# Kernel tuning notes

Measured on AMD Instinct MI355X. Metric: run time of the kernel, lower is better.

## Reference

```python
import jax, jax.numpy as jnp
import numpy as np

E = 64          # moe_num_experts
H = 1024        # hidden_size
F = 2816        # per_expert_ff_dim
T = 4096        # total tokens (equal split: 64 per expert)


def setup_inputs() -> dict:
    key = jax.random.key(0)
    k1, k2, k3, k4 = jax.random.split(key, 4)
    s = 1.0 / np.sqrt(H)
    return {
        "x": jax.random.normal(k1, (T, H), dtype=jnp.float32),
        "tokens_per_expert": jnp.full((E,), T // E, dtype=jnp.int32),
        "w1": jax.random.normal(k2, (E * F, H), dtype=jnp.float32) * s,
        "w3": jax.random.normal(k3, (E * F, H), dtype=jnp.float32) * s,
        "w2": jax.random.normal(k4, (E * F, H), dtype=jnp.float32) * s,
    }


def reference(x, tokens_per_expert, w1, w3, w2):
    # Tokens are grouped contiguously per expert with an equal split,
    # so the variable-size grouped GEMM (gg.ops.gmm) reduces to a batched einsum.
    tpe = x.shape[0] // E
    xg = x.reshape(E, tpe, H)            # [E, t, h]
    w1e = w1.reshape(E, F, H)
    w3e = w3.reshape(E, F, H)
    w2e = w2.reshape(E, F, H)
    # gmm(x, w1, trans_b=True): per-expert x @ w1[e].T
    h1 = jnp.einsum("eth,efh->etf", xg, w1e)   # [E, t, f]
    h3 = jnp.einsum("eth,efh->etf", xg, w3e)   # [E, t, f]
    gated = jax.nn.silu(h1) * h3               # SwiGLU
    # gmm(gated, w2): per-expert gated @ w2[e]  ([t,f] @ [f,h])
    out = jnp.einsum("etf,efh->eth", gated, w2e)
    return out.reshape(-1, H)
```

## Files before the change

kernel.cpp:

```cpp
#include <hip/hip_runtime.h>
#include <hip/hip_bf16.h>

#define NE   64
#define NH   1024
#define NF   2816
#define TPE  64
#define PITCH 72

typedef __attribute__((ext_vector_type(8))) short bf16x8;
typedef __attribute__((ext_vector_type(4))) float f32x4;

__device__ __forceinline__ ushort f2bf(float f) {
    union { float f; unsigned u; } v; v.f = f;
    unsigned r = v.u + 0x7fffu + ((v.u >> 16) & 1u);
    return (ushort)(r >> 16);
}

__device__ __forceinline__ bf16x8 cvt8(f32x4 lo, f32x4 hi) {
    bf16x8 r;
    #pragma unroll
    for (int j = 0; j < 4; ++j) {
        r[j]     = (short)f2bf(lo[j]);
        r[4 + j] = (short)f2bf(hi[j]);
    }
    return r;
}

#define GLOAD16(gsrc, ldst)                                                          \
    __builtin_amdgcn_global_load_lds(                                                \
        (const __attribute__((address_space(1))) void*)(gsrc),                       \
        (__attribute__((address_space(3))) void*)(ldst), 16, 0, 0)

__global__ __launch_bounds__(256)
void xcast(const float* __restrict__ x, ushort* __restrict__ xb) {
    const int i = blockIdx.x * 256 + threadIdx.x;
    const f32x4 a = *(const f32x4*)(x + (size_t)i * 8);
    const f32x4 b = *(const f32x4*)(x + (size_t)i * 8 + 4);
    *(bf16x8*)(xb + (size_t)i * 8) = cvt8(a, b);
}

__global__ __launch_bounds__(256, 4)
void k1_gate(const ushort* __restrict__ xb,
             const float* __restrict__ w1,
             const float* __restrict__ w3,
             ushort* __restrict__ g) {
    __shared__ float fbuf[10240];
    ushort* lX  = (ushort*)fbuf;
    float*  lW1 = fbuf + 2048;
    float*  lW3 = fbuf + 6144;

    const int e    = blockIdx.x;
    const int jt   = blockIdx.y;
    const int tid  = threadIdx.x;
    const int lane = tid & 63;
    const int wid  = tid >> 6;
    const int m15  = lane & 15;
    const int hi   = lane >> 4;
    const int mrow = wid * 16 + m15;

    const ushort* xA = xb + (size_t)e * TPE * NH;
    const float*  B1 = w1 + ((size_t)e * NF + (size_t)jt * 64) * NH;
    const float*  B3 = w3 + ((size_t)e * NF + (size_t)jt * 64) * NH;

    f32x4 acc1[4], acc3[4];
    #pragma unroll
    for (int nf = 0; nf < 4; ++nf) {
        acc1[nf] = f32x4{0.f, 0.f, 0.f, 0.f};
        acc3[nf] = f32x4{0.f, 0.f, 0.f, 0.f};
    }

    for (int kt = 0; kt < NH / 64; ++kt) {
        const size_t kb = (size_t)kt * 64;
        __syncthreads();
        #pragma unroll
        for (int i = 0; i < 2; ++i) {
            const int S   = i * 256 + tid;
            const int row = S >> 3;
            const int cs  = (S & 7) ^ (row & 7);
            GLOAD16(xA + (size_t)row * NH + kb + cs * 8, lX + (S & ~63) * 8);
        }
        #pragma unroll
        for (int i = 0; i < 4; ++i) {
            const int S   = i * 256 + tid;
            const int row = S >> 4;
            const int cs  = (S & 15) ^ (row & 15);
            const size_t goff = (size_t)row * NH + kb + cs * 4;
            GLOAD16(B1 + goff, lW1 + (S & ~63) * 4);
            GLOAD16(B3 + goff, lW3 + (S & ~63) * 4);
        }
        __syncthreads();

        #pragma unroll
        for (int ks = 0; ks < 2; ++ks) {
            const int sxa = ((ks * 4 + hi) ^ (mrow & 7)) << 3;
            const bf16x8 af = *(const bf16x8*)(lX + mrow * 64 + sxa);
            const int c0 = ks * 8 + hi * 2;
            #pragma unroll
            for (int nf = 0; nf < 4; ++nf) {
                const int brow = nf * 16 + m15;
                const int sa0 = (c0 ^ m15) << 2, sa1 = ((c0 + 1) ^ m15) << 2;
                const f32x4 p0 = *(const f32x4*)&lW1[brow * 64 + sa0];
                const f32x4 p1 = *(const f32x4*)&lW1[brow * 64 + sa1];
                acc1[nf] = __builtin_amdgcn_mfma_f32_16x16x32_bf16(af, cvt8(p0, p1), acc1[nf], 0, 0, 0);
                const f32x4 q0 = *(const f32x4*)&lW3[brow * 64 + sa0];
                const f32x4 q1 = *(const f32x4*)&lW3[brow * 64 + sa1];
                acc3[nf] = __builtin_amdgcn_mfma_f32_16x16x32_bf16(af, cvt8(q0, q1), acc3[nf], 0, 0, 0);
            }
        }
    }

    #pragma unroll
    for (int nf = 0; nf < 4; ++nf) {
        #pragma unroll
        for (int i = 0; i < 4; ++i) {
            const float h1v = acc1[nf][i];
            const float h3v = acc3[nf][i];
            const float s   = (h1v / (1.f + __expf(-h1v))) * h3v;
            const int row = wid * 16 + (hi * 4) + i;
            const int col = jt * 64 + nf * 16 + m15;
            const size_t t = (size_t)e * TPE + row;
            g[t * NF + col] = f2bf(s);
        }
    }
}

__global__ __launch_bounds__(256, 2)
void k2_down(const ushort* __restrict__ g,
             const float* __restrict__ w2,
             float* __restrict__ out) {
    __shared__ ushort lA[64 * PITCH];
    __shared__ ushort lB[64 * PITCH];

    const int jt   = blockIdx.x;
    const int e    = blockIdx.y;
    const int tid  = threadIdx.x;
    const int lane = tid & 63;
    const int wid  = tid >> 6;

    const ushort* A = g  + (size_t)e * TPE * NF;
    const float*  B = w2 + (size_t)e * NF * NH + (size_t)jt * 64;
    float* O = out + (size_t)e * TPE * NH + (size_t)jt * 64;

    f32x4 acc[4];
    for (int nf = 0; nf < 4; ++nf) acc[nf] = f32x4{0.f, 0.f, 0.f, 0.f};

    for (int kt = 0; kt < NF / 64; ++kt) {
        __syncthreads();
        #pragma unroll
        for (int r = 0; r < 2; ++r) {
            const int q   = tid + r * 256;
            const int row = q >> 3;
            const int k8  = (q & 7) * 8;
            *(bf16x8*)(&lA[row * PITCH + k8]) =
                *(const bf16x8*)(A + (size_t)row * NF + kt * 64 + k8);
        }
        {
            const int n  = tid & 63;
            const int kq = (tid >> 6) * 4;
            #pragma unroll
            for (int r = 0; r < 4; ++r) {
                const int ks = kq + r * 16;
                const size_t base = (size_t)(kt * 64 + ks) * NH + n;
                const float f0 = B[base];
                const float f1 = B[base + NH];
                const float f2 = B[base + 2 * (size_t)NH];
                const float f3 = B[base + 3 * (size_t)NH];
                ushort4 b;
                b.x = f2bf(f0); b.y = f2bf(f1); b.z = f2bf(f2); b.w = f2bf(f3);
                *(ushort4*)(&lB[n * PITCH + ks]) = b;
            }
        }
        __syncthreads();

        const int mrow = wid * 16 + (lane & 15);
        #pragma unroll
        for (int ks = 0; ks < 2; ++ks) {
            const int koff = ks * 32 + ((lane >> 4) * 8);
            const bf16x8 af = *(const bf16x8*)(&lA[mrow * PITCH + koff]);
            #pragma unroll
            for (int nf = 0; nf < 4; ++nf) {
                const bf16x8 bfr = *(const bf16x8*)(&lB[(nf * 16 + (lane & 15)) * PITCH + koff]);
                acc[nf] = __builtin_amdgcn_mfma_f32_16x16x32_bf16(af, bfr, acc[nf], 0, 0, 0);
            }
        }
    }

    #pragma unroll
    for (int nf = 0; nf < 4; ++nf) {
        #pragma unroll
        for (int i = 0; i < 4; ++i) {
            const int row = wid * 16 + ((lane >> 4) * 4) + i;
            const int col = nf * 16 + (lane & 15);
            O[(size_t)row * NH + col] = acc[nf][i];
        }
    }
}

extern "C" void kernel_launch(void* const* d_in, const int* in_sizes, int n_in,
                              void* d_out, int out_size, void* d_ws, size_t ws_size,
                              hipStream_t stream) {
    const float* x  = (const float*)d_in[0];
    const float* w1 = (const float*)d_in[2];
    const float* w3 = (const float*)d_in[3];
    const float* w2 = (const float*)d_in[4];
    float* out = (float*)d_out;
    ushort* gated = (ushort*)d_ws;
    ushort* xbf   = (ushort*)((char*)d_ws + (32u << 20));

    xcast<<<dim3((TPE * NE * NH) / (256 * 8)), dim3(256), 0, stream>>>(x, xbf);

    dim3 g1(NE, NF / 64);
    k1_gate<<<g1, dim3(256), 0, stream>>>(xbf, w1, w3, gated);

    dim3 g2(NH / 64, NE);
    k2_down<<<g2, dim3(256), 0, stream>>>(gated, w2, out);
}
```

Baseline: 456.4 us.

## Double-buffer k1_gate LDS loads with async prefetch two stages ahead

Converts the gate/up GEMM's k-loop into a two-stage double-buffered pipeline. Direct-to-LDS global loads for tile kt+2 are issued while tile kt is computed, with explicit vmcnt waits and raw barriers instead of __syncthreads. LDS use doubles to 80KB and launch bounds drop to 2 blocks per CU, trading occupancy for overlap. The grid is also transposed so consecutive blocks share an expert, which may improve locality of the x tile.

```diff
diff --git a/kernel.cpp b/kernel.cpp
--- a/kernel.cpp
+++ b/kernel.cpp
@@ -6,6 +6,7 @@
 #define NF   2816
 #define TPE  64
 #define PITCH 72
+#define K1BUF 10240
 
 typedef __attribute__((ext_vector_type(8))) short bf16x8;
 typedef __attribute__((ext_vector_type(4))) float f32x4;
@@ -39,18 +40,15 @@
     *(bf16x8*)(xb + (size_t)i * 8) = cvt8(a, b);
 }
 
-__global__ __launch_bounds__(256, 4)
+__global__ __launch_bounds__(256, 2)
 void k1_gate(const ushort* __restrict__ xb,
              const float* __restrict__ w1,
              const float* __restrict__ w3,
              ushort* __restrict__ g) {
-    __shared__ float fbuf[10240];
-    ushort* lX  = (ushort*)fbuf;
-    float*  lW1 = fbuf + 2048;
-    float*  lW3 = fbuf + 6144;
-
-    const int e    = blockIdx.x;
-    const int jt   = blockIdx.y;
+    __shared__ float fbuf[2 * K1BUF];
+
+    const int jt   = blockIdx.x;
+    const int e    = blockIdx.y;
     const int tid  = threadIdx.x;
     const int lane = tid & 63;
     const int wid  = tid >> 6;
@@ -69,45 +67,70 @@
         acc3[nf] = f32x4{0.f, 0.f, 0.f, 0.f};
     }
 
-    for (int kt = 0; kt < NH / 64; ++kt) {
-        const size_t kb = (size_t)kt * 64;
-        __syncthreads();
-        #pragma unroll
-        for (int i = 0; i < 2; ++i) {
-            const int S   = i * 256 + tid;
-            const int row = S >> 3;
-            const int cs  = (S & 7) ^ (row & 7);
-            GLOAD16(xA + (size_t)row * NH + kb + cs * 8, lX + (S & ~63) * 8);
-        }
-        #pragma unroll
-        for (int i = 0; i < 4; ++i) {
-            const int S   = i * 256 + tid;
-            const int row = S >> 4;
-            const int cs  = (S & 15) ^ (row & 15);
-            const size_t goff = (size_t)row * NH + kb + cs * 4;
-            GLOAD16(B1 + goff, lW1 + (S & ~63) * 4);
-            GLOAD16(B3 + goff, lW3 + (S & ~63) * 4);
-        }
-        __syncthreads();
+    #define STAGE(t, b)                                                              \
+        do {                                                                         \
+            float* bb = fbuf + (b) * K1BUF;                                          \
+            ushort* sX = (ushort*)bb;                                                \
+            float*  sW1 = bb + 2048;                                                 \
+            float*  sW3 = bb + 6144;                                                 \
+            const size_t kb = (size_t)(t) * 64;                                      \
+            _Pragma("unroll")                                                        \
+            for (int i = 0; i < 2; ++i) {                                            \
+                const int S   = i * 256 + tid;                                       \
+                const int row = S >> 3;                                              \
+                const int cs  = (S & 7) ^ (row & 7);                                 \
+                GLOAD16(xA + (size_t)row * NH + kb + cs * 8, sX + (S & ~63) * 8);    \
+            }                                                                        \
+            _Pragma("unroll")                                                        \
+            for (int i = 0; i < 4; ++i) {                                            \
+                const int S   = i * 256 + tid;                                       \
+                const int row = S >> 4;                                              \
+                const int cs  = (S & 15) ^ (row & 15);                               \
+                const size_t goff = (size_t)row * NH + kb + cs * 4;                  \
+                GLOAD16(B1 + goff, sW1 + (S & ~63) * 4);                             \
+                GLOAD16(B3 + goff, sW3 + (S & ~63) * 4);                             \
+            }                                                                        \
+        } while (0)
+
+    STAGE(0, 0);
+    STAGE(1, 1);
+
+    #pragma unroll
+    for (int kt = 0; kt < 16; ++kt) {
+        if (kt < 15) asm volatile("s_waitcnt vmcnt(10)" ::: "memory");
+        else         asm volatile("s_waitcnt vmcnt(0)"  ::: "memory");
+        __builtin_amdgcn_s_barrier();
+        asm volatile("" ::: "memory");
+
+        const float* bb = fbuf + (kt & 1) * K1BUF;
+        const ushort* sX = (const ushort*)bb;
+        const float*  sW1 = bb + 2048;
+        const float*  sW3 = bb + 6144;
 
         #pragma unroll
         for (int ks = 0; ks < 2; ++ks) {
             const int sxa = ((ks * 4 + hi) ^ (mrow & 7)) << 3;
-            const bf16x8 af = *(const bf16x8*)(lX + mrow * 64 + sxa);
+            const bf16x8 af = *(const bf16x8*)(sX + mrow * 64 + sxa);
             const int c0 = ks * 8 + hi * 2;
             #pragma unroll
             for (int nf = 0; nf < 4; ++nf) {
                 const int brow = nf * 16 + m15;
                 const int sa0 = (c0 ^ m15) << 2, sa1 = ((c0 + 1) ^ m15) << 2;
-                const f32x4 p0 = *(const f32x4*)&lW1[brow * 64 + sa0];
-                const f32x4 p1 = *(const f32x4*)&lW1[brow * 64 + sa1];
+                const f32x4 p0 = *(const f32x4*)&sW1[brow * 64 + sa0];
+                const f32x4 p1 = *(const f32x4*)&sW1[brow * 64 + sa1];
                 acc1[nf] = __builtin_amdgcn_mfma_f32_16x16x32_bf16(af, cvt8(p0, p1), acc1[nf], 0, 0, 0);
-                const f32x4 q0 = *(const f32x4*)&lW3[brow * 64 + sa0];
-                const f32x4 q1 = *(const f32x4*)&lW3[brow * 64 + sa1];
+                const f32x4 q0 = *(const f32x4*)&sW3[brow * 64 + sa0];
+                const f32x4 q1 = *(const f32x4*)&sW3[brow * 64 + sa1];
                 acc3[nf] = __builtin_amdgcn_mfma_f32_16x16x32_bf16(af, cvt8(q0, q1), acc3[nf], 0, 0, 0);
             }
         }
-    }
+
+        asm volatile("" ::: "memory");
+        __builtin_amdgcn_s_barrier();
+        asm volatile("" ::: "memory");
+        if (kt + 2 < 16) STAGE(kt + 2, kt & 1);
+    }
+    #undef STAGE
 
     #pragma unroll
     for (int nf = 0; nf < 4; ++nf) {
@@ -209,7 +232,7 @@
 
     xcast<<<dim3((TPE * NE * NH) / (256 * 8)), dim3(256), 0, stream>>>(x, xbf);
 
-    dim3 g1(NE, NF / 64);
+    dim3 g1(NF / 64, NE);
     k1_gate<<<g1, dim3(256), 0, stream>>>(xbf, w1, w3, gated);
 
     dim3 g2(NH / 64, NE);
```

Result: faster. 442.3 us (median of 2 runs) (-3.1%).

## Stage gate weights as bf16 in padded LDS, read activations directly from global

Applied to the files above, without the earlier changes.

The gate kernel stops using async global-to-LDS copies of fp32 weights and XOR-swizzled layouts. It now loads the fp32 w1/w3 tiles into registers, converts them to bf16 once, and stores them in padded LDS rows. The X fragment is read straight from global memory instead of being staged in LDS. The grid is transposed so consecutive blocks share an expert, and the occupancy hint drops from 4 to 2. This removes the per-MFMA fp32-to-bf16 conversion repeated by every wave and halves the LDS footprint, but it loses the async copy path and exposes global-load latency on the X reads.

```diff
diff --git a/kernel.cpp b/kernel.cpp
--- a/kernel.cpp
+++ b/kernel.cpp
@@ -25,11 +25,6 @@
     }
     return r;
 }
-
-#define GLOAD16(gsrc, ldst)                                                          \
-    __builtin_amdgcn_global_load_lds(                                                \
-        (const __attribute__((address_space(1))) void*)(gsrc),                       \
-        (__attribute__((address_space(3))) void*)(ldst), 16, 0, 0)
 
 __global__ __launch_bounds__(256)
 void xcast(const float* __restrict__ x, ushort* __restrict__ xb) {
@@ -39,18 +34,16 @@
     *(bf16x8*)(xb + (size_t)i * 8) = cvt8(a, b);
 }
 
-__global__ __launch_bounds__(256, 4)
+__global__ __launch_bounds__(256, 2)
 void k1_gate(const ushort* __restrict__ xb,
              const float* __restrict__ w1,
              const float* __restrict__ w3,
              ushort* __restrict__ g) {
-    __shared__ float fbuf[10240];
-    ushort* lX  = (ushort*)fbuf;
-    float*  lW1 = fbuf + 2048;
-    float*  lW3 = fbuf + 6144;
-
-    const int e    = blockIdx.x;
-    const int jt   = blockIdx.y;
+    __shared__ ushort lW1[64 * PITCH];
+    __shared__ ushort lW3[64 * PITCH];
+
+    const int jt   = blockIdx.x;
+    const int e    = blockIdx.y;
     const int tid  = threadIdx.x;
     const int lane = tid & 63;
     const int wid  = tid >> 6;
@@ -58,7 +51,7 @@
     const int hi   = lane >> 4;
     const int mrow = wid * 16 + m15;
 
-    const ushort* xA = xb + (size_t)e * TPE * NH;
+    const ushort* xA = xb + (size_t)e * TPE * NH + (size_t)mrow * NH;
     const float*  B1 = w1 + ((size_t)e * NF + (size_t)jt * 64) * NH;
     const float*  B3 = w3 + ((size_t)e * NF + (size_t)jt * 64) * NH;
 
@@ -69,42 +62,37 @@
         acc3[nf] = f32x4{0.f, 0.f, 0.f, 0.f};
     }
 
+    const int srow = tid >> 4;
+    const int sc4  = (tid & 15) * 4;
+
     for (int kt = 0; kt < NH / 64; ++kt) {
         const size_t kb = (size_t)kt * 64;
         __syncthreads();
         #pragma unroll
-        for (int i = 0; i < 2; ++i) {
-            const int S   = i * 256 + tid;
-            const int row = S >> 3;
-            const int cs  = (S & 7) ^ (row & 7);
-            GLOAD16(xA + (size_t)row * NH + kb + cs * 8, lX + (S & ~63) * 8);
-        }
-        #pragma unroll
-        for (int i = 0; i < 4; ++i) {
-            const int S   = i * 256 + tid;
-            const int row = S >> 4;
-            const int cs  = (S & 15) ^ (row & 15);
-            const size_t goff = (size_t)row * NH + kb + cs * 4;
-            GLOAD16(B1 + goff, lW1 + (S & ~63) * 4);
-            GLOAD16(B3 + goff, lW3 + (S & ~63) * 4);
+        for (int r = 0; r < 4; ++r) {
+            const int row = srow + r * 16;
+            const size_t goff = (size_t)row * NH + kb + sc4;
+            const float4 v1 = *(const float4*)(B1 + goff);
+            const float4 v3 = *(const float4*)(B3 + goff);
+            ushort4 u1, u3;
+            u1.x = f2bf(v1.x); u1.y = f2bf(v1.y); u1.z = f2bf(v1.z); u1.w = f2bf(v1.w);
+            u3.x = f2bf(v3.x); u3.y = f2bf(v3.y); u3.z = f2bf(v3.z); u3.w = f2bf(v3.w);
+            *(ushort4*)(&lW1[row * PITCH + sc4]) = u1;
+            *(ushort4*)(&lW3[row * PITCH + sc4]) = u3;
         }
         __syncthreads();
 
         #pragma unroll
         for (int ks = 0; ks < 2; ++ks) {
-            const int sxa = ((ks * 4 + hi) ^ (mrow & 7)) << 3;
-            const bf16x8 af = *(const bf16x8*)(lX + mrow * 64 + sxa);
-            const int c0 = ks * 8 + hi * 2;
+            const int koff = ks * 32 + hi * 8;
+            const bf16x8 af = *(const bf16x8*)(xA + kb + koff);
             #pragma unroll
             for (int nf = 0; nf < 4; ++nf) {
-                const int brow = nf * 16 + m15;
-                const int sa0 = (c0 ^ m15) << 2, sa1 = ((c0 + 1) ^ m15) << 2;
-                const f32x4 p0 = *(const f32x4*)&lW1[brow * 64 + sa0];
-                const f32x4 p1 = *(const f32x4*)&lW1[brow * 64 + sa1];
-                acc1[nf] = __builtin_amdgcn_mfma_f32_16x16x32_bf16(af, cvt8(p0, p1), acc1[nf], 0, 0, 0);
-                const f32x4 q0 = *(const f32x4*)&lW3[brow * 64 + sa0];
-                const f32x4 q1 = *(const f32x4*)&lW3[brow * 64 + sa1];
-                acc3[nf] = __builtin_amdgcn_mfma_f32_16x16x32_bf16(af, cvt8(q0, q1), acc3[nf], 0, 0, 0);
+                const int bo = (nf * 16 + m15) * PITCH + koff;
+                const bf16x8 b1 = *(const bf16x8*)(&lW1[bo]);
+                acc1[nf] = __builtin_amdgcn_mfma_f32_16x16x32_bf16(af, b1, acc1[nf], 0, 0, 0);
+                const bf16x8 b3 = *(const bf16x8*)(&lW3[bo]);
+                acc3[nf] = __builtin_amdgcn_mfma_f32_16x16x32_bf16(af, b3, acc3[nf], 0, 0, 0);
             }
         }
     }
@@ -209,7 +197,7 @@
 
     xcast<<<dim3((TPE * NE * NH) / (256 * 8)), dim3(256), 0, stream>>>(x, xbf);
 
-    dim3 g1(NE, NF / 64);
+    dim3 g1(NF / 64, NE);
     k1_gate<<<g1, dim3(256), 0, stream>>>(xbf, w1, w3, gated);
 
     dim3 g2(NH / 64, NE);
```

Measured after the change: 518.4 us. 1.14x slower.
